# Kernel tuning notes

Measured on AMD Instinct MI355X. Metric: run time of the kernel, lower is better.

## Reference

```python
import jax, jax.numpy as jnp
import numpy as np

B, P, D, H, K = 2, 4096, 128, 4, 16
HD = D // H


def _build_mask(key):
    # diagonal (self) + up to K random neighbors per asset, like set_neighborhoods
    nb = jax.random.randint(key, (P, K), 0, P)
    mask = jnp.zeros((P, P), dtype=bool)
    rows = jnp.arange(P)
    mask = mask.at[rows, rows].set(True)
    mask = mask.at[rows[:, None], nb].set(True)
    return mask


def setup_inputs() -> dict:
    key = jax.random.key(0)
    kx, kq, kk, kv, ko, kn = jax.random.split(key, 6)
    s = 1.0 / np.sqrt(D)
    return {
        "x": jax.random.normal(kx, (B, P, D), dtype=jnp.float32),
        "Wq": jax.random.normal(kq, (D, D), dtype=jnp.float32) * s,
        "Wk": jax.random.normal(kk, (D, D), dtype=jnp.float32) * s,
        "Wv": jax.random.normal(kv, (D, D), dtype=jnp.float32) * s,
        "Wo": jax.random.normal(ko, (D, D), dtype=jnp.float32) * s,
        "mask": _build_mask(kn),
    }


def reference(x, Wq, Wk, Wv, Wo, mask):
    b, p, d = x.shape
    # nn.Linear applies x @ W.T
    q = jnp.einsum("bpd,ed->bpe", x, Wq).reshape(b, p, H, HD).transpose(0, 2, 1, 3)
    k = jnp.einsum("bpd,ed->bpe", x, Wk).reshape(b, p, H, HD).transpose(0, 2, 1, 3)
    v = jnp.einsum("bpd,ed->bpe", x, Wv).reshape(b, p, H, HD).transpose(0, 2, 1, 3)
    scale = jnp.float32(HD) ** 0.5
    scores = jnp.einsum("bhpd,bhqd->bhpq", q, k) / scale  # [B,H,P,P]
    scores = jnp.where(mask[None, None, :, :], scores, -jnp.inf)
    w = jax.nn.softmax(scores, axis=-1)
    w = jnp.nan_to_num(w, nan=0.0)  # rows with no neighbors -> zeros
    ctx = jnp.einsum("bhpq,bhqd->bhpd", w, v)
    ctx = ctx.transpose(0, 2, 1, 3).reshape(b, p, d)
    return jnp.einsum("bpd,ed->bpe", ctx, Wo)
```

## Files before the change

### kernel.cpp

```cpp
#include <hip/hip_runtime.h>
#include <hip/hip_bf16.h>

#define PP     4096
#define BB     2
#define DD     128
#define NH     4
#define HDIM   32
#define MROWS  8192
#define MAXN   24

typedef __attribute__((ext_vector_type(8))) short short8;
typedef __attribute__((ext_vector_type(4))) float floatx4;

__device__ __forceinline__ unsigned short f2bf(float f) {
  __hip_bfloat16 h = __float2bfloat16(f);
  return *reinterpret_cast<unsigned short*>(&h);
}
__device__ __forceinline__ float bf2f(unsigned short u) {
  union { unsigned int i; float f; } c;
  c.i = ((unsigned int)u) << 16;
  return c.f;
}

__device__ __forceinline__ int detect_mode(const unsigned char* mask) {
  bool u8ok = true;
#pragma unroll
  for (int p = 1; p <= 3; ++p) {
    size_t f = (size_t)p * PP + p;
    u8ok = u8ok && (mask[f] == 1);
  }
  return u8ok ? 0 : 1;
}

__global__ void compact_kernel(const void* __restrict__ mask,
                               const float4* __restrict__ Wq,
                               const float4* __restrict__ Wk,
                               const float4* __restrict__ Wv,
                               const float4* __restrict__ Wo,
                               int* __restrict__ nbr_idx,
                               int* __restrict__ nbr_cnt,
                               unsigned short* __restrict__ Wb) {
  int p = blockIdx.x;
  int t = threadIdx.x;
  int lane = t & 63, wv = t >> 6;

  if (p < 64) {
    int u = p * 256 + t;
    int m = u >> 12, off = u & 4095;
    const float4* Ws = m == 0 ? Wq : (m == 1 ? Wk : (m == 2 ? Wv : Wo));
    float4 v = Ws[off];
    ushort4 o;
    o.x = f2bf(v.x); o.y = f2bf(v.y); o.z = f2bf(v.z); o.w = f2bf(v.w);
    *reinterpret_cast<ushort4*>(Wb + (size_t)m * DD * DD + (size_t)off * 4) = o;
  }

  int md = detect_mode((const unsigned char*)mask);
  unsigned int bits = 0;

  if (md == 0) {
    uint4 v = reinterpret_cast<const uint4*>((const unsigned char*)mask +
                                             (size_t)p * PP)[t];
    unsigned int w4[4] = {v.x, v.y, v.z, v.w};
#pragma unroll
    for (int wi = 0; wi < 4; ++wi) {
      unsigned int w = w4[wi];
      unsigned int nz = ((((w & 0x7F7F7F7Fu) + 0x7F7F7F7Fu) | w) & 0x80808080u);
      unsigned int x = (nz >> 7) & 0x01010101u;
      unsigned int b4 = (x | (x >> 7) | (x >> 14) | (x >> 21)) & 0xFu;
      bits |= b4 << (wi * 4);
    }
  } else {
    const uint4* base =
        reinterpret_cast<const uint4*>((const unsigned int*)mask + (size_t)p * PP) +
        t * 4;
#pragma unroll
    for (int c = 0; c < 4; ++c) {
      uint4 v = base[c];
      unsigned int b4 = (v.x ? 1u : 0u) | (v.y ? 2u : 0u) |
                        (v.z ? 4u : 0u) | (v.w ? 8u : 0u);
      bits |= b4 << (c * 4);
    }
  }

  int cnt = __popc(bits);
  int pre = cnt;
#pragma unroll
  for (int d = 1; d < 64; d <<= 1) {
    int tt = __shfl_up(pre, d);
    if (lane >= d) pre += tt;
  }
  __shared__ int wsum[4];
  if (lane == 63) wsum[wv] = pre;
  __syncthreads();
  int woff = 0;
#pragma unroll
  for (int w = 0; w < 4; ++w)
    if (w < wv) woff += wsum[w];
  int base_pos = woff + pre - cnt;
  unsigned int m = bits;
  while (m) {
    int b = __ffs(m) - 1;
    m &= m - 1;
    if (base_pos < MAXN) nbr_idx[p * MAXN + base_pos] = t * 16 + b;
    ++base_pos;
  }
  int total = wsum[0] + wsum[1] + wsum[2] + wsum[3];
  int cl = total < MAXN ? total : MAXN;
  if (t == 0) nbr_cnt[p] = cl;
  if (t >= cl && t < MAXN) nbr_idx[p * MAXN + t] = p;
}

__global__ void qkv_kernel(const float* __restrict__ x,
                           const unsigned short* __restrict__ Wb,
                           float* __restrict__ Qf,
                           unsigned short* __restrict__ Kb,
                           unsigned short* __restrict__ Vb) {
  int tid = threadIdx.x;
  int wv = tid >> 6;
  int lane = tid & 63;
  int lrow = lane & 15;
  int kb = lane >> 4;
  int row0 = blockIdx.x * 16;

  floatx4 acc[3][2];
#pragma unroll
  for (int m = 0; m < 3; ++m)
#pragma unroll
    for (int c = 0; c < 2; ++c) acc[m][c] = (floatx4){0.f, 0.f, 0.f, 0.f};

#pragma unroll
  for (int ks = 0; ks < 4; ++ks) {
    int k0 = ks * 32 + kb * 8;
    const float4* xr = reinterpret_cast<const float4*>(x + (size_t)(row0 + lrow) * DD + k0);
    float4 x0 = xr[0], x1 = xr[1];
    short8 a;
    a[0] = (short)f2bf(x0.x); a[1] = (short)f2bf(x0.y);
    a[2] = (short)f2bf(x0.z); a[3] = (short)f2bf(x0.w);
    a[4] = (short)f2bf(x1.x); a[5] = (short)f2bf(x1.y);
    a[6] = (short)f2bf(x1.z); a[7] = (short)f2bf(x1.w);
#pragma unroll
    for (int m = 0; m < 3; ++m) {
      const unsigned short* W = Wb + (size_t)m * DD * DD;
#pragma unroll
      for (int c = 0; c < 2; ++c) {
        int col_tile = wv * 2 + c;
        short8 bf = *reinterpret_cast<const short8*>(
            W + (size_t)(col_tile * 16 + lrow) * DD + k0);
        acc[m][c] = __builtin_amdgcn_mfma_f32_16x16x32_bf16(a, bf, acc[m][c], 0, 0, 0);
      }
    }
  }
#pragma unroll
  for (int c = 0; c < 2; ++c)
#pragma unroll
    for (int r = 0; r < 4; ++r) {
      size_t off = (size_t)(row0 + kb * 4 + r) * DD + (wv * 2 + c) * 16 + lrow;
      Qf[off] = acc[0][c][r];
      Kb[off] = f2bf(acc[1][c][r]);
      Vb[off] = f2bf(acc[2][c][r]);
    }
}

__global__ void attn_kernel(const float* __restrict__ Qf,
                            const unsigned short* __restrict__ Kb,
                            const unsigned short* __restrict__ Vb,
                            const int* __restrict__ nbr_idx,
                            const int* __restrict__ nbr_cnt,
                            unsigned short* __restrict__ ctxb) {
  int tid = threadIdx.x;
  int r = tid >> 7;
  int sub = tid & 127;
  int h = sub >> 5, il = sub & 31;
  int row = blockIdx.x * 2 + r;
  int b = row >> 12;
  int bBase = b * PP;

  __shared__ int idx_s[2][MAXN];
  __shared__ int cnt_s[2];
  __shared__ float ws_s[2][NH][32];
  if (tid < 2) cnt_s[tid] = nbr_cnt[(blockIdx.x * 2 + tid) & (PP - 1)];
  if (tid >= 128 && tid < 128 + 2 * MAXN) {
    int u = tid - 128;
    idx_s[u / MAXN][u % MAXN] =
        nbr_idx[((blockIdx.x * 2 + u / MAXN) & (PP - 1)) * MAXN + u % MAXN];
  }
  __syncthreads();
  int cnt = cnt_s[r];

  int slot = il < MAXN ? il : MAXN - 1;
  int j = idx_s[r][slot];
  const unsigned short* Kr = Kb + (size_t)(bBase + j) * DD + h * HDIM;
  const float4* Qr = reinterpret_cast<const float4*>(Qf + (size_t)row * DD + h * HDIM);
  float acc = 0.f;
#pragma unroll
  for (int c = 0; c < 4; ++c) {
    short8 kk = *reinterpret_cast<const short8*>(Kr + c * 8);
    float4 q0 = Qr[c * 2], q1 = Qr[c * 2 + 1];
    acc = fmaf(q0.x, bf2f((unsigned short)kk[0]), acc);
    acc = fmaf(q0.y, bf2f((unsigned short)kk[1]), acc);
    acc = fmaf(q0.z, bf2f((unsigned short)kk[2]), acc);
    acc = fmaf(q0.w, bf2f((unsigned short)kk[3]), acc);
    acc = fmaf(q1.x, bf2f((unsigned short)kk[4]), acc);
    acc = fmaf(q1.y, bf2f((unsigned short)kk[5]), acc);
    acc = fmaf(q1.z, bf2f((unsigned short)kk[6]), acc);
    acc = fmaf(q1.w, bf2f((unsigned short)kk[7]), acc);
  }
  float s = (il < cnt) ? acc * 0.17677669529663689f : -1e30f;

  float mx = s;
  mx = fmaxf(mx, __shfl_xor(mx, 16));
  mx = fmaxf(mx, __shfl_xor(mx, 8));
  mx = fmaxf(mx, __shfl_xor(mx, 4));
  mx = fmaxf(mx, __shfl_xor(mx, 2));
  mx = fmaxf(mx, __shfl_xor(mx, 1));
  float w = (il < cnt) ? __expf(s - mx) : 0.f;
  float l = w;
  l += __shfl_xor(l, 16);
  l += __shfl_xor(l, 8);
  l += __shfl_xor(l, 4);
  l += __shfl_xor(l, 2);
  l += __shfl_xor(l, 1);
  ws_s[r][h][il] = w / l;
  __syncthreads();

  float acc2 = 0.f;
#pragma unroll
  for (int i = 0; i < MAXN; ++i) {
    int jj = idx_s[r][i];
    float wgt = ws_s[r][h][i];
    acc2 = fmaf(wgt, bf2f(Vb[(size_t)(bBase + jj) * DD + h * HDIM + il]), acc2);
  }
  ctxb[(size_t)row * DD + h * HDIM + il] = f2bf(acc2);
}

__global__ void oproj_kernel(const unsigned short* __restrict__ ctxb,
                             const unsigned short* __restrict__ WoB,
                             float* __restrict__ out) {
  int tid = threadIdx.x;
  int wv = tid >> 6;
  int lane = tid & 63;
  int lrow = lane & 15;
  int kb = lane >> 4;
  int row0 = blockIdx.x * 16;

  floatx4 acc[2];
  acc[0] = (floatx4){0.f, 0.f, 0.f, 0.f};
  acc[1] = (floatx4){0.f, 0.f, 0.f, 0.f};
#pragma unroll
  for (int ks = 0; ks < 4; ++ks) {
    int k0 = ks * 32 + kb * 8;
    short8 a = *reinterpret_cast<const short8*>(ctxb + (size_t)(row0 + lrow) * DD + k0);
#pragma unroll
    for (int c = 0; c < 2; ++c) {
      int col_tile = wv * 2 + c;
      short8 bf = *reinterpret_cast<const short8*>(
          WoB + (size_t)(col_tile * 16 + lrow) * DD + k0);
      acc[c] = __builtin_amdgcn_mfma_f32_16x16x32_bf16(a, bf, acc[c], 0, 0, 0);
    }
  }
#pragma unroll
  for (int c = 0; c < 2; ++c)
#pragma unroll
    for (int r = 0; r < 4; ++r)
      out[(size_t)(row0 + kb * 4 + r) * DD + (wv * 2 + c) * 16 + lrow] = acc[c][r];
}

extern "C" void kernel_launch(void* const* d_in, const int* in_sizes, int n_in,
                              void* d_out, int out_size, void* d_ws, size_t ws_size,
                              hipStream_t stream) {
  const float* x    = (const float*)d_in[0];
  const float* Wq   = (const float*)d_in[1];
  const float* Wk   = (const float*)d_in[2];
  const float* Wv   = (const float*)d_in[3];
  const float* Wo   = (const float*)d_in[4];
  const void*  mask = d_in[5];
  float* out = (float*)d_out;

  char* ws = (char*)d_ws;
  int* nbr_cnt = (int*)(ws + 0);
  int* nbr_idx = (int*)(ws + 16384);
  unsigned short* Wb = (unsigned short*)(ws + 409600);
  float* Qf = (float*)(ws + 540672);
  unsigned short* Kb = (unsigned short*)(ws + 4734976);
  unsigned short* Vb = (unsigned short*)(ws + 6832128);
  unsigned short* ctxb = (unsigned short*)(ws + 8929280);

  compact_kernel<<<PP, 256, 0, stream>>>(mask, (const float4*)Wq, (const float4*)Wk,
                                         (const float4*)Wv, (const float4*)Wo,
                                         nbr_idx, nbr_cnt, Wb);
  qkv_kernel<<<MROWS / 16, 256, 0, stream>>>(x, Wb, Qf, Kb, Vb);
  attn_kernel<<<MROWS / 2, 256, 0, stream>>>(Qf, Kb, Vb, nbr_idx, nbr_cnt, ctxb);
  oproj_kernel<<<MROWS / 16, 256, 0, stream>>>(ctxb, Wb + (size_t)3 * DD * DD, out);
}
```

Baseline: 46.75 us.

## Fuse mask compaction with QKV projection and drop weight pre-conversion

Merges the mask-compaction kernel and the QKV projection into one launch, using a block-index split: the first 512 blocks do the QKV GEMM and the rest compact the mask. Weights are no longer pre-converted to bf16 in a separate pass. Both the QKV and output-projection kernels now load fp32 weights and convert them per fragment in registers. This removes one kernel launch and the dependency between the weight conversion and the GEMM, at the cost of twice the weight-load bytes and redundant conversion work in every block.

```diff
diff --git a/kernel.cpp b/kernel.cpp
--- a/kernel.cpp
+++ b/kernel.cpp
@@ -8,6 +8,7 @@
 #define HDIM   32
 #define MROWS  8192
 #define MAXN   24
+#define QKVB   512
 
 typedef __attribute__((ext_vector_type(8))) short short8;
 typedef __attribute__((ext_vector_type(4))) float floatx4;
@@ -22,6 +23,17 @@
   return c.f;
 }
 
+__device__ __forceinline__ short8 load_frag_f32(const float* p) {
+  const float4* p4 = reinterpret_cast<const float4*>(p);
+  float4 a = p4[0], b = p4[1];
+  short8 r;
+  r[0] = (short)f2bf(a.x); r[1] = (short)f2bf(a.y);
+  r[2] = (short)f2bf(a.z); r[3] = (short)f2bf(a.w);
+  r[4] = (short)f2bf(b.x); r[5] = (short)f2bf(b.y);
+  r[6] = (short)f2bf(b.z); r[7] = (short)f2bf(b.w);
+  return r;
+}
+
 __device__ __forceinline__ int detect_mode(const unsigned char* mask) {
   bool u8ok = true;
 #pragma unroll
@@ -32,28 +44,58 @@
   return u8ok ? 0 : 1;
 }
 
-__global__ void compact_kernel(const void* __restrict__ mask,
-                               const float4* __restrict__ Wq,
-                               const float4* __restrict__ Wk,
-                               const float4* __restrict__ Wv,
-                               const float4* __restrict__ Wo,
-                               int* __restrict__ nbr_idx,
-                               int* __restrict__ nbr_cnt,
-                               unsigned short* __restrict__ Wb) {
-  int p = blockIdx.x;
+__global__ void fused_compact_qkv(const void* __restrict__ mask,
+                                  const float* __restrict__ x,
+                                  const float* __restrict__ Wq,
+                                  const float* __restrict__ Wk,
+                                  const float* __restrict__ Wv,
+                                  int* __restrict__ nbr_idx,
+                                  int* __restrict__ nbr_cnt,
+                                  float* __restrict__ Qf,
+                                  unsigned short* __restrict__ Kb,
+                                  unsigned short* __restrict__ Vb) {
   int t = threadIdx.x;
   int lane = t & 63, wv = t >> 6;
 
-  if (p < 64) {
-    int u = p * 256 + t;
-    int m = u >> 12, off = u & 4095;
-    const float4* Ws = m == 0 ? Wq : (m == 1 ? Wk : (m == 2 ? Wv : Wo));
-    float4 v = Ws[off];
-    ushort4 o;
-    o.x = f2bf(v.x); o.y = f2bf(v.y); o.z = f2bf(v.z); o.w = f2bf(v.w);
-    *reinterpret_cast<ushort4*>(Wb + (size_t)m * DD * DD + (size_t)off * 4) = o;
-  }
-
+  if (blockIdx.x < QKVB) {
+    int lrow = lane & 15;
+    int kb = lane >> 4;
+    int row0 = blockIdx.x * 16;
+
+    floatx4 acc[3][2];
+#pragma unroll
+    for (int m = 0; m < 3; ++m)
+#pragma unroll
+      for (int c = 0; c < 2; ++c) acc[m][c] = (floatx4){0.f, 0.f, 0.f, 0.f};
+
+#pragma unroll
+    for (int ks = 0; ks < 4; ++ks) {
+      int k0 = ks * 32 + kb * 8;
+      short8 a = load_frag_f32(x + (size_t)(row0 + lrow) * DD + k0);
+#pragma unroll
+      for (int m = 0; m < 3; ++m) {
+        const float* W = m == 0 ? Wq : (m == 1 ? Wk : Wv);
+#pragma unroll
+        for (int c = 0; c < 2; ++c) {
+          int col_tile = wv * 2 + c;
+          short8 bf = load_frag_f32(W + (size_t)(col_tile * 16 + lrow) * DD + k0);
+          acc[m][c] = __builtin_amdgcn_mfma_f32_16x16x32_bf16(a, bf, acc[m][c], 0, 0, 0);
+        }
+      }
+    }
+#pragma unroll
+    for (int c = 0; c < 2; ++c)
+#pragma unroll
+      for (int r = 0; r < 4; ++r) {
+        size_t off = (size_t)(row0 + kb * 4 + r) * DD + (wv * 2 + c) * 16 + lrow;
+        Qf[off] = acc[0][c][r];
+        Kb[off] = f2bf(acc[1][c][r]);
+        Vb[off] = f2bf(acc[2][c][r]);
+      }
+    return;
+  }
+
+  int p = blockIdx.x - QKVB;
   int md = detect_mode((const unsigned char*)mask);
   unsigned int bits = 0;
 
@@ -65,8 +107,8 @@
     for (int wi = 0; wi < 4; ++wi) {
       unsigned int w = w4[wi];
       unsigned int nz = ((((w & 0x7F7F7F7Fu) + 0x7F7F7F7Fu) | w) & 0x80808080u);
-      unsigned int x = (nz >> 7) & 0x01010101u;
-      unsigned int b4 = (x | (x >> 7) | (x >> 14) | (x >> 21)) & 0xFu;
+      unsigned int xbit = (nz >> 7) & 0x01010101u;
+      unsigned int b4 = (xbit | (xbit >> 7) | (xbit >> 14) | (xbit >> 21)) & 0xFu;
       bits |= b4 << (wi * 4);
     }
   } else {
@@ -108,57 +150,6 @@
   int cl = total < MAXN ? total : MAXN;
   if (t == 0) nbr_cnt[p] = cl;
   if (t >= cl && t < MAXN) nbr_idx[p * MAXN + t] = p;
-}
-
-__global__ void qkv_kernel(const float* __restrict__ x,
-                           const unsigned short* __restrict__ Wb,
-                           float* __restrict__ Qf,
-                           unsigned short* __restrict__ Kb,
-                           unsigned short* __restrict__ Vb) {
-  int tid = threadIdx.x;
-  int wv = tid >> 6;
-  int lane = tid & 63;
-  int lrow = lane & 15;
-  int kb = lane >> 4;
-  int row0 = blockIdx.x * 16;
-
-  floatx4 acc[3][2];
-#pragma unroll
-  for (int m = 0; m < 3; ++m)
-#pragma unroll
-    for (int c = 0; c < 2; ++c) acc[m][c] = (floatx4){0.f, 0.f, 0.f, 0.f};
-
-#pragma unroll
-  for (int ks = 0; ks < 4; ++ks) {
-    int k0 = ks * 32 + kb * 8;
-    const float4* xr = reinterpret_cast<const float4*>(x + (size_t)(row0 + lrow) * DD + k0);
-    float4 x0 = xr[0], x1 = xr[1];
-    short8 a;
-    a[0] = (short)f2bf(x0.x); a[1] = (short)f2bf(x0.y);
-    a[2] = (short)f2bf(x0.z); a[3] = (short)f2bf(x0.w);
-    a[4] = (short)f2bf(x1.x); a[5] = (short)f2bf(x1.y);
-    a[6] = (short)f2bf(x1.z); a[7] = (short)f2bf(x1.w);
-#pragma unroll
-    for (int m = 0; m < 3; ++m) {
-      const unsigned short* W = Wb + (size_t)m * DD * DD;
-#pragma unroll
-      for (int c = 0; c < 2; ++c) {
-        int col_tile = wv * 2 + c;
-        short8 bf = *reinterpret_cast<const short8*>(
-            W + (size_t)(col_tile * 16 + lrow) * DD + k0);
-        acc[m][c] = __builtin_amdgcn_mfma_f32_16x16x32_bf16(a, bf, acc[m][c], 0, 0, 0);
-      }
-    }
-  }
-#pragma unroll
-  for (int c = 0; c < 2; ++c)
-#pragma unroll
-    for (int r = 0; r < 4; ++r) {
-      size_t off = (size_t)(row0 + kb * 4 + r) * DD + (wv * 2 + c) * 16 + lrow;
-      Qf[off] = acc[0][c][r];
-      Kb[off] = f2bf(acc[1][c][r]);
-      Vb[off] = f2bf(acc[2][c][r]);
-    }
 }
 
 __global__ void attn_kernel(const float* __restrict__ Qf,
@@ -234,7 +225,7 @@
 }
 
 __global__ void oproj_kernel(const unsigned short* __restrict__ ctxb,
-                             const unsigned short* __restrict__ WoB,
+                             const float* __restrict__ Wo,
                              float* __restrict__ out) {
   int tid = threadIdx.x;
   int wv = tid >> 6;
@@ -253,8 +244,7 @@
 #pragma unroll
     for (int c = 0; c < 2; ++c) {
       int col_tile = wv * 2 + c;
-      short8 bf = *reinterpret_cast<const short8*>(
-          WoB + (size_t)(col_tile * 16 + lrow) * DD + k0);
+      short8 bf = load_frag_f32(Wo + (size_t)(col_tile * 16 + lrow) * DD + k0);
       acc[c] = __builtin_amdgcn_mfma_f32_16x16x32_bf16(a, bf, acc[c], 0, 0, 0);
     }
   }
@@ -279,16 +269,13 @@
   char* ws = (char*)d_ws;
   int* nbr_cnt = (int*)(ws + 0);
   int* nbr_idx = (int*)(ws + 16384);
-  unsigned short* Wb = (unsigned short*)(ws + 409600);
-  float* Qf = (float*)(ws + 540672);
-  unsigned short* Kb = (unsigned short*)(ws + 4734976);
-  unsigned short* Vb = (unsigned short*)(ws + 6832128);
-  unsigned short* ctxb = (unsigned short*)(ws + 8929280);
-
-  compact_kernel<<<PP, 256, 0, stream>>>(mask, (const float4*)Wq, (const float4*)Wk,
-                                         (const float4*)Wv, (const float4*)Wo,
-                                         nbr_idx, nbr_cnt, Wb);
-  qkv_kernel<<<MROWS / 16, 256, 0, stream>>>(x, Wb, Qf, Kb, Vb);
+  float* Qf = (float*)(ws + 409600);
+  unsigned short* Kb = (unsigned short*)(ws + 4603904);
+  unsigned short* Vb = (unsigned short*)(ws + 6701056);
+  unsigned short* ctxb = (unsigned short*)(ws + 8798208);
+
+  fused_compact_qkv<<<QKVB + PP, 256, 0, stream>>>(
+      mask, x, Wq, Wk, Wv, nbr_idx, nbr_cnt, Qf, Kb, Vb);
   attn_kernel<<<MROWS / 2, 256, 0, stream>>>(Qf, Kb, Vb, nbr_idx, nbr_cnt, ctxb);
-  oproj_kernel<<<MROWS / 16, 256, 0, stream>>>(ctxb, Wb + (size_t)3 * DD * DD, out);
-}
+  oproj_kernel<<<MROWS / 16, 256, 0, stream>>>(ctxb, Wo, out);
+}
```

After: 45.92 us. Within noise of the previous version (-1.8%).
